# Optimization experiments

Hardware: AMD Instinct MI355X
Metric: run time of the kernel (lower is better)

The kernel has to match this reference:

```python
import jax, jax.numpy as jnp
import numpy as np

N_NODES = 100000
IN_F = 256
OUT_F = 256
BATCH = 50000
NUM_SAMPLES = 25


def setup_inputs() -> dict:
    key = jax.random.key(0)
    k1, k2, k3, k4 = jax.random.split(key, 4)
    features = jax.random.normal(k1, (N_NODES, IN_F), dtype=jnp.float32)
    node_idx = jax.random.randint(k2, (BATCH,), 0, N_NODES, dtype=jnp.int64 if jax.config.jax_enable_x64 else jnp.int32)
    neigh_idx = jax.random.randint(k3, (BATCH, NUM_SAMPLES), 0, N_NODES, dtype=jnp.int64 if jax.config.jax_enable_x64 else jnp.int32)
    # Linear(2*in_features, out_features, bias=False); torch stores weight as [out, 2*in],
    # we store W as [out, 2*in] transposed to [2*in, out] for x @ W.
    init_range = np.sqrt(6.0 / (2 * IN_F + OUT_F))
    W = jax.random.uniform(k4, (OUT_F, 2 * IN_F), dtype=jnp.float32, minval=-init_range, maxval=init_range)
    return {"features": features, "node_idx": node_idx, "neigh_idx": neigh_idx, "W": W}


def reference(features, node_idx, neigh_idx, W):
    # self features: [B, in]
    self_feat = features[node_idx]
    # gather + mean over sampled neighbors: [B, S, in] -> [B, in]
    neigh_mean = jnp.mean(features[neigh_idx], axis=1)
    # concat and project: [B, 2*in] @ [2*in, out]
    combined = jnp.concatenate([self_feat, neigh_mean], axis=1)
    return combined @ W.T
```

## Files before the change

kernel.cpp:

```cpp
#include <hip/hip_runtime.h>

#define N_NODES 100000
#define IN_F    256
#define OUT_F   256
#define BATCH   50000
#define NSAMP   25
#define K2      512
#define BKH     128
#define NTILE   1563
#define XS      256

typedef _Float16 f16_t;
typedef f16_t f16x8 __attribute__((ext_vector_type(8)));
typedef float f32x4 __attribute__((ext_vector_type(4)));
typedef float f32x2 __attribute__((ext_vector_type(2)));
typedef __bf16 bf16_t;
typedef bf16_t bf16x8 __attribute__((ext_vector_type(8)));

#if defined(__has_builtin)
#if __has_builtin(__builtin_amdgcn_cvt_pk_f32_fp8) && __has_builtin(__builtin_amdgcn_cvt_pk_fp8_f32)
#define FP8_HW 1
#endif
#endif
#ifndef FP8_HW
#include <hip/hip_fp8.h>
#endif

#define P8_OFF   51200000L
#define WG_OFF   76800000L
#define WS_NEED  (WG_OFF + 512L * 256 * 2)

typedef __attribute__((address_space(1))) const unsigned int gas_uint;
typedef __attribute__((address_space(3))) unsigned int las_uint;

__device__ __forceinline__ void gll16(const void* g, void* l) {
    __builtin_amdgcn_global_load_lds((gas_uint*)g, (las_uint*)l, 16, 0, 0);
}

__device__ __forceinline__ float h2f(unsigned short u) {
    union { unsigned short u; f16_t h; } t; t.u = u; return (float)t.h;
}

__device__ __forceinline__ unsigned int pk_fp8x4(float a, float b, float c, float d) {
#ifdef FP8_HW
    unsigned int r = __builtin_amdgcn_cvt_pk_fp8_f32(a, b, 0u, false);
    r = __builtin_amdgcn_cvt_pk_fp8_f32(c, d, r, true);
    return r;
#else
    union { unsigned char b[4]; unsigned int u; } t;
    t.b[0] = __hip_fp8_e4m3(a).__x; t.b[1] = __hip_fp8_e4m3(b).__x;
    t.b[2] = __hip_fp8_e4m3(c).__x; t.b[3] = __hip_fp8_e4m3(d).__x;
    return t.u;
#endif
}

__device__ __forceinline__ void acc_fp8x4(unsigned int v, float4& a) {
#ifdef FP8_HW
    f32x2 lo = __builtin_amdgcn_cvt_pk_f32_fp8(v, false);
    f32x2 hi = __builtin_amdgcn_cvt_pk_f32_fp8(v, true);
    a.x += lo[0]; a.y += lo[1]; a.z += hi[0]; a.w += hi[1];
#else
    union { unsigned int u; unsigned char b[4]; } t; t.u = v;
    __hip_fp8_e4m3 e0, e1, e2, e3;
    e0.__x = t.b[0]; e1.__x = t.b[1]; e2.__x = t.b[2]; e3.__x = t.b[3];
    a.x += (float)e0; a.y += (float)e1; a.z += (float)e2; a.w += (float)e3;
#endif
}

__global__ void wconv(const float* __restrict__ W, f16_t* __restrict__ Wg) {
    int idx = blockIdx.x * 256 + threadIdx.x;
    int j = idx >> 8, k = idx & 255;
    float v = (j < 256) ? W[j * K2 + k] : W[(j - 256) * K2 + 256 + k];
    Wg[idx] = (f16_t)v;
}

__global__ __launch_bounds__(512, 2) void proj_gemm(
    const float* __restrict__ features, const f16_t* __restrict__ Wg,
    f16_t* __restrict__ Pself, unsigned char* __restrict__ Pneigh8)
{
    __shared__ float buf[2][64 * BKH];
    const int tid = threadIdx.x, lane = tid & 63, w = tid >> 6;
    const int q16 = lane >> 4, r16 = lane & 15;
    const int c0 = blockIdx.y * 256 + w * 32;

    f16x8 wgall[8][2];
    #pragma unroll
    for (int s = 0; s < 8; ++s)
        #pragma unroll
        for (int ct = 0; ct < 2; ++ct)
            wgall[s][ct] = *(const f16x8*)&Wg[(long)(c0 + ct * 16 + r16) * 256 + s * 32 + q16 * 8];

    f32x4 acc[2][4];
    #pragma unroll
    for (int ct = 0; ct < 2; ++ct)
        #pragma unroll
        for (int rt = 0; rt < 4; ++rt) acc[ct][rt] = (f32x4){0.f, 0.f, 0.f, 0.f};

#define STAGE(TT, HH, BSEL)                                                     \
    {                                                                           \
        const long gr_ = (long)(TT) * 64;                                       \
        _Pragma("unroll")                                                       \
        for (int i_ = 0; i_ < 4; ++i_) {                                        \
            const int c_ = w * 4 + i_;                                          \
            const int row_ = 2 * c_ + (lane >> 5);                              \
            long srow_ = gr_ + row_; if (srow_ > N_NODES - 1) srow_ = N_NODES - 1; \
            const int sg4_ = ((lane & 31) ^ (row_ & 7)) * 4;                    \
            gll16(&features[srow_ * IN_F + (HH) * BKH + sg4_],                  \
                  &buf[BSEL][c_ * 256]);                                        \
        }                                                                       \
    }

    STAGE(blockIdx.x, 0, 0);
    int cur = 0;

    for (int t = blockIdx.x; t < NTILE; t += XS) {
        #pragma unroll
        for (int h = 0; h < 2; ++h) {
            __builtin_amdgcn_s_barrier();
            const int nt = (h == 0) ? t : t + XS;
            const bool hn = nt < NTILE;
            if (hn) {
                STAGE(nt, h ^ 1, cur ^ 1);
                asm volatile("s_waitcnt vmcnt(4)" ::: "memory");
            } else {
                asm volatile("s_waitcnt vmcnt(0)" ::: "memory");
            }
            __builtin_amdgcn_sched_barrier(0);
            __builtin_amdgcn_s_barrier();

            #pragma unroll
            for (int sl = 0; sl < 4; ++sl) {
                const int sg = h * 4 + sl;
                f16x8 bfr[4];
                #pragma unroll
                for (int rt = 0; rt < 4; ++rt) {
                    const int row = rt * 16 + r16;
                    const int lg0 = sl * 8 + q16 * 2;
                    const float4 lo = *(const float4*)
                        &buf[cur][row * BKH + ((lg0 ^ (row & 7)) << 2)];
                    const float4 hi = *(const float4*)
                        &buf[cur][row * BKH + (((lg0 + 1) ^ (row & 7)) << 2)];
                    f16x8 bb;
                    bb[0] = (f16_t)lo.x; bb[1] = (f16_t)lo.y;
                    bb[2] = (f16_t)lo.z; bb[3] = (f16_t)lo.w;
                    bb[4] = (f16_t)hi.x; bb[5] = (f16_t)hi.y;
                    bb[6] = (f16_t)hi.z; bb[7] = (f16_t)hi.w;
                    bfr[rt] = bb;
                }
                #pragma unroll
                for (int ct = 0; ct < 2; ++ct)
                    #pragma unroll
                    for (int rt = 0; rt < 4; ++rt)
                        acc[ct][rt] = __builtin_amdgcn_mfma_f32_16x16x32_f16(
                            wgall[sg][ct], bfr[rt], acc[ct][rt], 0, 0, 0);
            }
            cur ^= 1;
        }

        const long gr0 = (long)t * 64;
        if (blockIdx.y == 0) {
            #pragma unroll
            for (int rt = 0; rt < 4; ++rt) {
                const long row = gr0 + rt * 16 + r16;
                const bool ok = row < N_NODES;
                #pragma unroll
                for (int ct = 0; ct < 2; ++ct) {
                    const int colb = w * 32 + ct * 16 + q16 * 4;
                    if (ok) {
                        union { ushort4 u; f16_t hh[4]; } tt;
                        tt.hh[0] = (f16_t)acc[ct][rt][0]; tt.hh[1] = (f16_t)acc[ct][rt][1];
                        tt.hh[2] = (f16_t)acc[ct][rt][2]; tt.hh[3] = (f16_t)acc[ct][rt][3];
                        *(ushort4*)&Pself[row * 256 + colb] = tt.u;
                    }
                }
            }
        } else {
            #pragma unroll
            for (int rt = 0; rt < 4; ++rt) {
                const long row = gr0 + rt * 16 + r16;
                const bool ok = row < N_NODES;
                #pragma unroll
                for (int ct = 0; ct < 2; ++ct) {
                    const int colb = w * 32 + ct * 16 + q16 * 4;
                    unsigned int pk = pk_fp8x4(acc[ct][rt][0], acc[ct][rt][1],
                                               acc[ct][rt][2], acc[ct][rt][3]);
                    if (ok) *(unsigned int*)&Pneigh8[row * 256 + colb] = pk;
                }
            }
        }
        #pragma unroll
        for (int ct = 0; ct < 2; ++ct)
            #pragma unroll
            for (int rt = 0; rt < 4; ++rt) acc[ct][rt] = (f32x4){0.f, 0.f, 0.f, 0.f};
    }
#undef STAGE
}

__global__ __launch_bounds__(256) void gather_add(
    const f16_t* __restrict__ Pself, const unsigned char* __restrict__ P8,
    const int* __restrict__ node_idx, const int* __restrict__ neigh_idx,
    float* __restrict__ out)
{
    const int tid = threadIdx.x, lane = tid & 63, w = tid >> 6;
    const long b0 = (long)blockIdx.x * 8 + w * 2;
    const int c4 = lane * 4;

    int ns0[NSAMP], ns1[NSAMP];
    #pragma unroll
    for (int s = 0; s < NSAMP; ++s) ns0[s] = neigh_idx[b0 * NSAMP + s];
    #pragma unroll
    for (int s = 0; s < NSAMP; ++s) ns1[s] = neigh_idx[(b0 + 1) * NSAMP + s];
    const int sn0 = node_idx[b0], sn1 = node_idx[b0 + 1];

    const ushort4 sv0 = *(const ushort4*)&Pself[(long)sn0 * 256 + c4];
    const ushort4 sv1 = *(const ushort4*)&Pself[(long)sn1 * 256 + c4];

    unsigned int v0[NSAMP], v1[NSAMP];
    #pragma unroll
    for (int s = 0; s < NSAMP; ++s)
        v0[s] = *(const unsigned int*)&P8[(long)ns0[s] * 256 + c4];
    #pragma unroll
    for (int s = 0; s < NSAMP; ++s)
        v1[s] = *(const unsigned int*)&P8[(long)ns1[s] * 256 + c4];

    float4 a0 = make_float4(0.f, 0.f, 0.f, 0.f);
    float4 a1 = make_float4(0.f, 0.f, 0.f, 0.f);
    #pragma unroll
    for (int s = 0; s < NSAMP; ++s) acc_fp8x4(v0[s], a0);
    #pragma unroll
    for (int s = 0; s < NSAMP; ++s) acc_fp8x4(v1[s], a1);

    const float inv = 1.0f / (float)NSAMP;
    float4 o0, o1;
    o0.x = h2f(sv0.x) + a0.x * inv; o0.y = h2f(sv0.y) + a0.y * inv;
    o0.z = h2f(sv0.z) + a0.z * inv; o0.w = h2f(sv0.w) + a0.w * inv;
    o1.x = h2f(sv1.x) + a1.x * inv; o1.y = h2f(sv1.y) + a1.y * inv;
    o1.z = h2f(sv1.z) + a1.z * inv; o1.w = h2f(sv1.w) + a1.w * inv;
    *(float4*)&out[b0 * OUT_F + c4] = o0;
    *(float4*)&out[(b0 + 1) * OUT_F + c4] = o1;
}

__device__ __forceinline__ int swz_bf(int row, int us_idx) {
    return us_idx ^ ((row & 7) << 3);
}
__device__ __forceinline__ void store_bf4(unsigned short* comb, int r, int col, float4 f) {
    union { ushort4 u; bf16_t b[4]; } t;
    t.b[0] = (bf16_t)f.x; t.b[1] = (bf16_t)f.y;
    t.b[2] = (bf16_t)f.z; t.b[3] = (bf16_t)f.w;
    *(ushort4*)&comb[swz_bf(r, r * K2 + col)] = t.u;
}
__global__ __launch_bounds__(256, 4) void sage_fused(
    const float* __restrict__ features, const int* __restrict__ node_idx,
    const int* __restrict__ neigh_idx, const float* __restrict__ W,
    float* __restrict__ out)
{
    __shared__ unsigned short comb[16 * K2];
    const int tid = threadIdx.x, lane = tid & 63, wy = tid >> 6;
    const int b0 = blockIdx.x * 16;
    const int col4 = lane * 4;
    #pragma unroll
    for (int i = 0; i < 4; ++i) {
        const int r = wy * 4 + i;
        const long b = b0 + r;
        int nidx[NSAMP];
        #pragma unroll
        for (int s = 0; s < NSAMP; ++s) nidx[s] = neigh_idx[b * NSAMP + s];
        const int self_n = node_idx[b];
        const float4 sf = *(const float4*)&features[(long)self_n * IN_F + col4];
        float4 v[13];
        #pragma unroll
        for (int s = 0; s < 13; ++s)
            v[s] = *(const float4*)&features[(long)nidx[s] * IN_F + col4];
        float4 acc = v[0];
        #pragma unroll
        for (int s = 1; s < 13; ++s) {
            acc.x += v[s].x; acc.y += v[s].y; acc.z += v[s].z; acc.w += v[s].w;
        }
        #pragma unroll
        for (int s = 13; s < NSAMP; ++s)
            v[s - 13] = *(const float4*)&features[(long)nidx[s] * IN_F + col4];
        #pragma unroll
        for (int s = 0; s < 12; ++s) {
            acc.x += v[s].x; acc.y += v[s].y; acc.z += v[s].z; acc.w += v[s].w;
        }
        const float inv = 1.0f / (float)NSAMP;
        acc.x *= inv; acc.y *= inv; acc.z *= inv; acc.w *= inv;
        store_bf4(comb, r, col4, sf);
        store_bf4(comb, r, IN_F + col4, acc);
    }
    __syncthreads();
    const int c0 = wy * 64, arow = lane & 15, kq = (lane >> 4) * 8;
    f32x4 acc[4];
    #pragma unroll
    for (int t = 0; t < 4; ++t) acc[t] = (f32x4){0.f, 0.f, 0.f, 0.f};
    #pragma unroll
    for (int ks = 0; ks < 16; ++ks) {
        const int kb = ks * 32 + kq;
        const bf16x8 af = *(const bf16x8*)&comb[swz_bf(arow, arow * K2 + kb)];
        #pragma unroll
        for (int t = 0; t < 4; ++t) {
            const float* wp = &W[(long)(c0 + t * 16 + arow) * K2 + kb];
            const float4 w0 = *(const float4*)wp;
            const float4 w1 = *(const float4*)(wp + 4);
            bf16x8 bf;
            bf[0] = (bf16_t)w0.x; bf[1] = (bf16_t)w0.y;
            bf[2] = (bf16_t)w0.z; bf[3] = (bf16_t)w0.w;
            bf[4] = (bf16_t)w1.x; bf[5] = (bf16_t)w1.y;
            bf[6] = (bf16_t)w1.z; bf[7] = (bf16_t)w1.w;
            acc[t] = __builtin_amdgcn_mfma_f32_16x16x32_bf16(af, bf, acc[t], 0, 0, 0);
        }
    }
    #pragma unroll
    for (int t = 0; t < 4; ++t) {
        const int col = c0 + t * 16 + arow;
        #pragma unroll
        for (int j = 0; j < 4; ++j) {
            const int row = b0 + (lane >> 4) * 4 + j;
            out[(long)row * OUT_F + col] = acc[t][j];
        }
    }
}

extern "C" void kernel_launch(void* const* d_in, const int* in_sizes, int n_in,
                              void* d_out, int out_size, void* d_ws, size_t ws_size,
                              hipStream_t stream) {
    const float* features  = (const float*)d_in[0];
    const int*   node_idx  = (const int*)d_in[1];
    const int*   neigh_idx = (const int*)d_in[2];
    const float* W         = (const float*)d_in[3];
    float*       out       = (float*)d_out;

    if (ws_size >= (size_t)WS_NEED) {
        f16_t*         Pself  = (f16_t*)d_ws;
        unsigned char* P8     = (unsigned char*)d_ws + P8_OFF;
        f16_t*         Wg     = (f16_t*)((char*)d_ws + WG_OFF);
        wconv<<<512, 256, 0, stream>>>(W, Wg);
        proj_gemm<<<dim3(XS, 2), 512, 0, stream>>>(features, Wg, Pself, P8);
        gather_add<<<BATCH / 8, 256, 0, stream>>>(Pself, P8, node_idx, neigh_idx, out);
    } else {
        sage_fused<<<BATCH / 16, 256, 0, stream>>>(features, node_idx, neigh_idx, W, out);
    }
}
```

Measured before the change: 135.6 us.

## Stage projection tiles through registers as fp16 instead of direct-to-LDS fp32

```diff
diff --git a/kernel.cpp b/kernel.cpp
--- a/kernel.cpp
+++ b/kernel.cpp
@@ -6,7 +6,6 @@
 #define BATCH   50000
 #define NSAMP   25
 #define K2      512
-#define BKH     128
 #define NTILE   1563
 #define XS      256
 
@@ -29,13 +28,6 @@
 #define P8_OFF   51200000L
 #define WG_OFF   76800000L
 #define WS_NEED  (WG_OFF + 512L * 256 * 2)
-
-typedef __attribute__((address_space(1))) const unsigned int gas_uint;
-typedef __attribute__((address_space(3))) unsigned int las_uint;
-
-__device__ __forceinline__ void gll16(const void* g, void* l) {
-    __builtin_amdgcn_global_load_lds((gas_uint*)g, (las_uint*)l, 16, 0, 0);
-}
 
 __device__ __forceinline__ float h2f(unsigned short u) {
     union { unsigned short u; f16_t h; } t; t.u = u; return (float)t.h;
@@ -78,10 +70,12 @@
     const float* __restrict__ features, const f16_t* __restrict__ Wg,
     f16_t* __restrict__ Pself, unsigned char* __restrict__ Pneigh8)
 {
-    __shared__ float buf[2][64 * BKH];
+    __shared__ unsigned short buf[2][64 * 256];
     const int tid = threadIdx.x, lane = tid & 63, w = tid >> 6;
     const int q16 = lane >> 4, r16 = lane & 15;
     const int c0 = blockIdx.y * 256 + w * 32;
+    const int row_s = tid >> 3;
+    const int seg_s = tid & 7;
 
     f16x8 wgall[8][2];
     #pragma unroll
@@ -96,65 +90,51 @@
         #pragma unroll
         for (int rt = 0; rt < 4; ++rt) acc[ct][rt] = (f32x4){0.f, 0.f, 0.f, 0.f};
 
-#define STAGE(TT, HH, BSEL)                                                     \
+    float4 v[8];
+
+#define VLOAD(TT)                                                               \
     {                                                                           \
-        const long gr_ = (long)(TT) * 64;                                       \
+        long sr_ = (long)(TT) * 64 + row_s;                                     \
+        if (sr_ > N_NODES - 1) sr_ = N_NODES - 1;                               \
+        const float* p_ = &features[sr_ * IN_F + seg_s * 32];                   \
         _Pragma("unroll")                                                       \
-        for (int i_ = 0; i_ < 4; ++i_) {                                        \
-            const int c_ = w * 4 + i_;                                          \
-            const int row_ = 2 * c_ + (lane >> 5);                              \
-            long srow_ = gr_ + row_; if (srow_ > N_NODES - 1) srow_ = N_NODES - 1; \
-            const int sg4_ = ((lane & 31) ^ (row_ & 7)) * 4;                    \
-            gll16(&features[srow_ * IN_F + (HH) * BKH + sg4_],                  \
-                  &buf[BSEL][c_ * 256]);                                        \
-        }                                                                       \
-    }
-
-    STAGE(blockIdx.x, 0, 0);
+        for (int j_ = 0; j_ < 8; ++j_) v[j_] = *(const float4*)(p_ + j_ * 4);   \
+    }
+
+    VLOAD(blockIdx.x);
     int cur = 0;
 
     for (int t = blockIdx.x; t < NTILE; t += XS) {
         #pragma unroll
-        for (int h = 0; h < 2; ++h) {
-            __builtin_amdgcn_s_barrier();
-            const int nt = (h == 0) ? t : t + XS;
-            const bool hn = nt < NTILE;
-            if (hn) {
-                STAGE(nt, h ^ 1, cur ^ 1);
-                asm volatile("s_waitcnt vmcnt(4)" ::: "memory");
-            } else {
-                asm volatile("s_waitcnt vmcnt(0)" ::: "memory");
+        for (int p = 0; p < 4; ++p) {
+            const int g  = seg_s * 4 + p;
+            const int gp = g ^ (row_s & 7);
+            f16x8 hh;
+            hh[0] = (f16_t)v[2 * p].x;     hh[1] = (f16_t)v[2 * p].y;
+            hh[2] = (f16_t)v[2 * p].z;     hh[3] = (f16_t)v[2 * p].w;
+            hh[4] = (f16_t)v[2 * p + 1].x; hh[5] = (f16_t)v[2 * p + 1].y;
+            hh[6] = (f16_t)v[2 * p + 1].z; hh[7] = (f16_t)v[2 * p + 1].w;
+            *(f16x8*)&buf[cur][row_s * 256 + gp * 8] = hh;
+        }
+        __syncthreads();
+
+        if (t + XS < NTILE) VLOAD(t + XS);
+
+        #pragma unroll
+        for (int sg = 0; sg < 8; ++sg) {
+            f16x8 bfr[4];
+            #pragma unroll
+            for (int rt = 0; rt < 4; ++rt) {
+                const int row = rt * 16 + r16;
+                const int g   = (sg * 4 + q16) ^ (row & 7);
+                bfr[rt] = *(const f16x8*)&buf[cur][row * 256 + g * 8];
             }
-            __builtin_amdgcn_sched_barrier(0);
-            __builtin_amdgcn_s_barrier();
-
-            #pragma unroll
-            for (int sl = 0; sl < 4; ++sl) {
-                const int sg = h * 4 + sl;
-                f16x8 bfr[4];
+            #pragma unroll
+            for (int ct = 0; ct < 2; ++ct)
                 #pragma unroll
-                for (int rt = 0; rt < 4; ++rt) {
-                    const int row = rt * 16 + r16;
-                    const int lg0 = sl * 8 + q16 * 2;
-                    const float4 lo = *(const float4*)
-                        &buf[cur][row * BKH + ((lg0 ^ (row & 7)) << 2)];
-                    const float4 hi = *(const float4*)
-                        &buf[cur][row * BKH + (((lg0 + 1) ^ (row & 7)) << 2)];
-                    f16x8 bb;
-                    bb[0] = (f16_t)lo.x; bb[1] = (f16_t)lo.y;
-                    bb[2] = (f16_t)lo.z; bb[3] = (f16_t)lo.w;
-                    bb[4] = (f16_t)hi.x; bb[5] = (f16_t)hi.y;
-                    bb[6] = (f16_t)hi.z; bb[7] = (f16_t)hi.w;
-                    bfr[rt] = bb;
-                }
-                #pragma unroll
-                for (int ct = 0; ct < 2; ++ct)
-                    #pragma unroll
-                    for (int rt = 0; rt < 4; ++rt)
-                        acc[ct][rt] = __builtin_amdgcn_mfma_f32_16x16x32_f16(
-                            wgall[sg][ct], bfr[rt], acc[ct][rt], 0, 0, 0);
-            }
-            cur ^= 1;
+                for (int rt = 0; rt < 4; ++rt)
+                    acc[ct][rt] = __builtin_amdgcn_mfma_f32_16x16x32_f16(
+                        wgall[sg][ct], bfr[rt], acc[ct][rt], 0, 0, 0);
         }
 
         const long gr0 = (long)t * 64;
@@ -192,8 +172,9 @@
         for (int ct = 0; ct < 2; ++ct)
             #pragma unroll
             for (int rt = 0; rt < 4; ++rt) acc[ct][rt] = (f32x4){0.f, 0.f, 0.f, 0.f};
-    }
-#undef STAGE
+        cur ^= 1;
+    }
+#undef VLOAD
 }
 
 __global__ __launch_bounds__(256) void gather_add(
```

After: 124.8 us, median of 2. 1.09x faster.

## Pre-convert features to fp16 and stage full-K fp16 tiles in GEMM

Applied to the files above, without the earlier changes.

```diff
diff --git a/kernel.cpp b/kernel.cpp
--- a/kernel.cpp
+++ b/kernel.cpp
@@ -6,7 +6,6 @@
 #define BATCH   50000
 #define NSAMP   25
 #define K2      512
-#define BKH     128
 #define NTILE   1563
 #define XS      256
 
@@ -67,6 +66,19 @@
 #endif
 }
 
+__global__ __launch_bounds__(256) void fcvt(const float* __restrict__ F,
+                                            f16_t* __restrict__ F16) {
+    const long n4 = (long)N_NODES * IN_F / 4;
+    for (long i = (long)blockIdx.x * 256 + threadIdx.x; i < n4;
+         i += (long)gridDim.x * 256) {
+        float4 f = *(const float4*)&F[i * 4];
+        union { ushort4 u; f16_t h[4]; } t;
+        t.h[0] = (f16_t)f.x; t.h[1] = (f16_t)f.y;
+        t.h[2] = (f16_t)f.z; t.h[3] = (f16_t)f.w;
+        *(ushort4*)&F16[i * 4] = t.u;
+    }
+}
+
 __global__ void wconv(const float* __restrict__ W, f16_t* __restrict__ Wg) {
     int idx = blockIdx.x * 256 + threadIdx.x;
     int j = idx >> 8, k = idx & 255;
@@ -75,10 +87,10 @@
 }
 
 __global__ __launch_bounds__(512, 2) void proj_gemm(
-    const float* __restrict__ features, const f16_t* __restrict__ Wg,
+    const f16_t* __restrict__ F16, const f16_t* __restrict__ Wg,
     f16_t* __restrict__ Pself, unsigned char* __restrict__ Pneigh8)
 {
-    __shared__ float buf[2][64 * BKH];
+    __shared__ unsigned short buf[2][64 * 256];
     const int tid = threadIdx.x, lane = tid & 63, w = tid >> 6;
     const int q16 = lane >> 4, r16 = lane & 15;
     const int c0 = blockIdx.y * 256 + w * 32;
@@ -96,65 +108,53 @@
         #pragma unroll
         for (int rt = 0; rt < 4; ++rt) acc[ct][rt] = (f32x4){0.f, 0.f, 0.f, 0.f};
 
-#define STAGE(TT, HH, BSEL)                                                     \
+#define STAGE(TT, BSEL)                                                         \
     {                                                                           \
         const long gr_ = (long)(TT) * 64;                                       \
         _Pragma("unroll")                                                       \
         for (int i_ = 0; i_ < 4; ++i_) {                                        \
-            const int c_ = w * 4 + i_;                                          \
+            const int c_ = w * 4 + i_;                         \
             const int row_ = 2 * c_ + (lane >> 5);                              \
             long srow_ = gr_ + row_; if (srow_ > N_NODES - 1) srow_ = N_NODES - 1; \
-            const int sg4_ = ((lane & 31) ^ (row_ & 7)) * 4;                    \
-            gll16(&features[srow_ * IN_F + (HH) * BKH + sg4_],                  \
-                  &buf[BSEL][c_ * 256]);                                        \
+            const int g8_ = (((lane & 31) ^ (row_ & 7)) * 8);   \
+            gll16(&F16[srow_ * 256 + g8_], &buf[BSEL][c_ * 512]);               \
         }                                                                       \
     }
 
-    STAGE(blockIdx.x, 0, 0);
+    STAGE(blockIdx.x, 0);
     int cur = 0;
+    bool first = true;
 
     for (int t = blockIdx.x; t < NTILE; t += XS) {
-        #pragma unroll
-        for (int h = 0; h < 2; ++h) {
-            __builtin_amdgcn_s_barrier();
-            const int nt = (h == 0) ? t : t + XS;
-            const bool hn = nt < NTILE;
-            if (hn) {
-                STAGE(nt, h ^ 1, cur ^ 1);
-                asm volatile("s_waitcnt vmcnt(4)" ::: "memory");
-            } else {
-                asm volatile("s_waitcnt vmcnt(0)" ::: "memory");
+        __builtin_amdgcn_s_barrier();
+        const int nt = t + XS;
+        const bool hn = nt < NTILE;
+        if (hn) {
+            STAGE(nt, cur ^ 1);
+            if (first) asm volatile("s_waitcnt vmcnt(4)" ::: "memory");
+            else       asm volatile("s_waitcnt vmcnt(12)" ::: "memory");
+        } else {
+            asm volatile("s_waitcnt vmcnt(8)" ::: "memory");
+        }
+        __builtin_amdgcn_sched_barrier(0);
+        __builtin_amdgcn_s_barrier();
+        first = false;
+
+        #pragma unroll
+        for (int sg = 0; sg < 8; ++sg) {
+            f16x8 bfr[4];
+            #pragma unroll
+            for (int rt = 0; rt < 4; ++rt) {
+                const int row = rt * 16 + r16;
+                const int g   = (sg * 4 + q16) ^ (row & 7);
+                bfr[rt] = *(const f16x8*)&buf[cur][row * 256 + g * 8];
             }
-            __builtin_amdgcn_sched_barrier(0);
-            __builtin_amdgcn_s_barrier();
-
-            #pragma unroll
-            for (int sl = 0; sl < 4; ++sl) {
-                const int sg = h * 4 + sl;
-                f16x8 bfr[4];
+            #pragma unroll
+            for (int ct = 0; ct < 2; ++ct)
                 #pragma unroll
-                for (int rt = 0; rt < 4; ++rt) {
-                    const int row = rt * 16 + r16;
-                    const int lg0 = sl * 8 + q16 * 2;
-                    const float4 lo = *(const float4*)
-                        &buf[cur][row * BKH + ((lg0 ^ (row & 7)) << 2)];
-                    const float4 hi = *(const float4*)
-                        &buf[cur][row * BKH + (((lg0 + 1) ^ (row & 7)) << 2)];
-                    f16x8 bb;
-                    bb[0] = (f16_t)lo.x; bb[1] = (f16_t)lo.y;
-                    bb[2] = (f16_t)lo.z; bb[3] = (f16_t)lo.w;
-                    bb[4] = (f16_t)hi.x; bb[5] = (f16_t)hi.y;
-                    bb[6] = (f16_t)hi.z; bb[7] = (f16_t)hi.w;
-                    bfr[rt] = bb;
-                }
-                #pragma unroll
-                for (int ct = 0; ct < 2; ++ct)
-                    #pragma unroll
-                    for (int rt = 0; rt < 4; ++rt)
-                        acc[ct][rt] = __builtin_amdgcn_mfma_f32_16x16x32_f16(
-                            wgall[sg][ct], bfr[rt], acc[ct][rt], 0, 0, 0);
-            }
-            cur ^= 1;
+                for (int rt = 0; rt < 4; ++rt)
+                    acc[ct][rt] = __builtin_amdgcn_mfma_f32_16x16x32_f16(
+                        wgall[sg][ct], bfr[rt], acc[ct][rt], 0, 0, 0);
         }
 
         const long gr0 = (long)t * 64;
@@ -192,6 +192,7 @@
         for (int ct = 0; ct < 2; ++ct)
             #pragma unroll
             for (int rt = 0; rt < 4; ++rt) acc[ct][rt] = (f32x4){0.f, 0.f, 0.f, 0.f};
+        cur ^= 1;
     }
 #undef STAGE
 }
@@ -334,8 +335,10 @@
         f16_t*         Pself  = (f16_t*)d_ws;
         unsigned char* P8     = (unsigned char*)d_ws + P8_OFF;
         f16_t*         Wg     = (f16_t*)((char*)d_ws + WG_OFF);
+        f16_t*         F16    = (f16_t*)d_out;
+        fcvt<<<2048, 256, 0, stream>>>(features, F16);
         wconv<<<512, 256, 0, stream>>>(W, Wg);
-        proj_gemm<<<dim3(XS, 2), 512, 0, stream>>>(features, Wg, Pself, P8);
+        proj_gemm<<<dim3(XS, 2), 512, 0, stream>>>(F16, Wg, Pself, P8);
         gather_add<<<BATCH / 8, 256, 0, stream>>>(Pself, P8, node_idx, neigh_idx, out);
     } else {
         sage_fused<<<BATCH / 16, 256, 0, stream>>>(features, node_idx, neigh_idx, W, out);
```

Result: faster. 125.8 us (-7.3%).
